# Kernel optimization log

Hardware: AMD Instinct MI355X
Metric: run time of the kernel (lower is better)

Reference implementation:

```python
import jax, jax.numpy as jnp
import numpy as np
import math

B_ = 4
L_ = 2048
D_MODEL = 1024
D_STATE = 128
D_CONV = 4
HEADDIM = 64
CHUNK = 256
D_INNER = 2 * D_MODEL
NHEADS = D_INNER // HEADDIM
CONV_DIM = D_INNER + 2 * D_STATE
D_IN_PROJ = 2 * D_INNER + 2 * D_STATE + NHEADS


def setup_inputs() -> dict:
    key = jax.random.key(0)
    ks = jax.random.split(key, 8)
    u = jax.random.normal(ks[0], (B_, L_, D_MODEL), jnp.float32)
    W_in = jax.random.normal(ks[1], (D_IN_PROJ, D_MODEL), jnp.float32) * 0.02
    conv_w = jax.random.normal(ks[2], (CONV_DIM, D_CONV), jnp.float32) * 0.2
    conv_b = jnp.zeros((CONV_DIM,), jnp.float32)
    # dt init as in the torch module: dt ~ logU(0.001, 0.1), inverse-softplus
    dt = jnp.exp(jax.random.uniform(ks[3], (NHEADS,), jnp.float32) * (math.log(0.1) - math.log(0.001)) + math.log(0.001))
    dt = jnp.clip(dt, 1e-4, None)
    dt_bias = dt + jnp.log(-jnp.expm1(-dt))
    A_log = jnp.log(jax.random.uniform(ks[4], (NHEADS,), jnp.float32, minval=1.0, maxval=1.1))
    D_param = jnp.ones((NHEADS,), jnp.float32)
    norm_w = jnp.ones((D_INNER,), jnp.float32)
    W_out = jax.random.normal(ks[5], (D_MODEL, D_INNER), jnp.float32) * 0.02
    return {"u": u, "W_in": W_in, "conv_w": conv_w, "conv_b": conv_b,
            "dt_bias": dt_bias, "A_log": A_log, "D_param": D_param,
            "norm_w": norm_w, "W_out": W_out}


def _ssd(x, dt, A, Bm, Cm):
    """Chunked SSD scan (mamba_chunk_scan_combined math, ngroups=1).
    x: (b,l,h,p)  dt: (b,l,h) post-softplus  A: (h,)  Bm/Cm: (b,l,n)."""
    b, l, h, p = x.shape
    n = Bm.shape[-1]
    nc = l // CHUNK
    xr = x.reshape(b, nc, CHUNK, h, p)
    dtr = dt.reshape(b, nc, CHUNK, h)
    Br = Bm.reshape(b, nc, CHUNK, n)
    Cr = Cm.reshape(b, nc, CHUNK, n)
    dA = dtr * A                                    # (b,nc,cs,h), negative
    dA_cs = jnp.cumsum(dA, axis=2)                  # (b,nc,cs,h)
    # intra-chunk decay L[i,j] = exp(sum_{k=j+1..i} dA_k) for i >= j else 0
    diff = dA_cs[:, :, :, None, :] - dA_cs[:, :, None, :, :]  # (b,nc,i,j,h)
    mask = jnp.tril(jnp.ones((CHUNK, CHUNK), bool))
    Lmat = jnp.exp(jnp.where(mask[None, None, :, :, None], diff, -jnp.inf))
    dtx = dtr[..., None] * xr                       # (b,nc,cs,h,p)
    Y_diag = jnp.einsum('bcin,bcjn,bcijh,bcjhp->bcihp', Cr, Br, Lmat, dtx)
    # per-chunk final states
    decay_states = jnp.exp(dA_cs[:, :, -1:, :] - dA_cs)  # (b,nc,cs,h)
    states = jnp.einsum('bcjn,bcjh,bcjhp->bchpn', Br, decay_states, dtx)
    # inter-chunk recurrence over nc
    chunk_decay = jnp.exp(dA_cs[:, :, -1, :])       # (b,nc,h)
    def step(carry, inp):
        s, d = inp
        return carry * d[:, :, None, None] + s, carry
    init = jnp.zeros((b, h, p, n), x.dtype)
    _, prev = jax.lax.scan(step, init, (jnp.moveaxis(states, 1, 0), jnp.moveaxis(chunk_decay, 1, 0)))
    prev = jnp.moveaxis(prev, 0, 1)                 # (b,nc,h,p,n): state entering each chunk
    Y_off = jnp.einsum('bcin,bchpn,bcih->bcihp', Cr, prev, jnp.exp(dA_cs))
    return (Y_diag + Y_off).reshape(b, l, h, p)


def reference(u, W_in, conv_w, conv_b, dt_bias, A_log, D_param, norm_w, W_out):
    b, l, _ = u.shape
    zxbcdt = jnp.einsum('bld,ed->ble', u, W_in)     # (b,l,d_in_proj)
    z = zxbcdt[..., :D_INNER]
    xBC = zxbcdt[..., D_INNER:D_INNER + CONV_DIM]
    dt = zxbcdt[..., D_INNER + CONV_DIM:]
    # depthwise causal conv1d + SiLU
    xt = jnp.moveaxis(xBC, 1, 2)                    # (b,c,l)
    y = jax.lax.conv_general_dilated(xt, conv_w[:, None, :], (1,), [(D_CONV - 1, 0)], feature_group_count=CONV_DIM)
    xBC = jax.nn.silu(jnp.moveaxis(y + conv_b[None, :, None], 2, 1))
    x = xBC[..., :D_INNER].reshape(b, l, NHEADS, HEADDIM)
    Bm = xBC[..., D_INNER:D_INNER + D_STATE]
    Cm = xBC[..., D_INNER + D_STATE:]
    dt = jax.nn.softplus(dt + dt_bias)
    A = -jnp.exp(A_log)
    yh = _ssd(x, dt, A, Bm, Cm) + D_param[:, None] * x
    yf = yh.reshape(b, l, D_INNER)
    # gated RMSNorm (norm_before_gate=False): norm(y * silu(z)) * w
    g = yf * jax.nn.silu(z)
    g = g * jax.lax.rsqrt(jnp.mean(g * g, axis=-1, keepdims=True) + 1e-5) * norm_w
    return jnp.einsum('bld,ed->ble', g, W_out)
```

## Files before the change

kernel.cpp:

```cpp
#include <hip/hip_runtime.h>
#include <hip/hip_bf16.h>
#include <math.h>

#define B_N     4
#define L_N     2048
#define DMODEL  1024
#define DSTATE  128
#define DCONV   4
#define HEADDIM 64
#define CHUNK   256
#define DINNER  2048
#define NHEADS  32
#define CONVDIM 2304
#define DINPROJ 4384
#define NCHUNK  8
#define BL      (B_N*L_N)

typedef unsigned short ushort_t;
typedef unsigned int   uint_t;

typedef __attribute__((ext_vector_type(8))) short bf16x8;
typedef __attribute__((ext_vector_type(4))) float f32x4;

__device__ __forceinline__ float bfbits2f(ushort_t u){
    union { uint_t i; float f; } v; v.i = ((uint_t)u) << 16; return v.f;
}
__device__ __forceinline__ ushort_t f2bf(float f){
    union { float f; uint_t i; } v; v.f = f;
    uint_t r = v.i + 0x7FFF + ((v.i >> 16) & 1);
    return (ushort_t)(r >> 16);
}
__device__ __forceinline__ void gload_lds16(const void* g, void* l){
    __builtin_amdgcn_global_load_lds(
        (const __attribute__((address_space(1))) unsigned int*)g,
        (__attribute__((address_space(3))) unsigned int*)l, 16, 0, 0);
}

__global__ __launch_bounds__(256) void cvt_bf16(
    const float* __restrict__ in, ushort_t* __restrict__ out, int n8)
{
    int i = blockIdx.x*256 + threadIdx.x;
    if (i >= n8) return;
    const float4* p = (const float4*)(in + (size_t)i*8);
    float4 a = p[0], b = p[1];
    ushort_t o[8] = { f2bf(a.x), f2bf(a.y), f2bf(a.z), f2bf(a.w),
                      f2bf(b.x), f2bf(b.y), f2bf(b.z), f2bf(b.w) };
    *(uint4*)(out + (size_t)i*8) = *(const uint4*)o;
}

__global__ __launch_bounds__(256) void cvt_wT(
    const float* __restrict__ cw, float* __restrict__ wT)
{
    int c = blockIdx.x*256 + threadIdx.x;
    if (c >= CONVDIM) return;
    float4 v = *(const float4*)&cw[c*DCONV];
    wT[0*CONVDIM + c] = v.x;
    wT[1*CONVDIM + c] = v.y;
    wT[2*CONVDIM + c] = v.z;
    wT[3*CONVDIM + c] = v.w;
}

template<int KDIM, int NTILES, int EPI>
__global__ __launch_bounds__(256) void gemm_bt_mfma(
    const ushort_t* __restrict__ A, const ushort_t* __restrict__ B,
    float* __restrict__ outf, ushort_t* __restrict__ z, ushort_t* __restrict__ xbc,
    const float* __restrict__ dt_bias, float* __restrict__ dtp)
{
    __shared__ __align__(16) ushort_t Asl[2][128*32];
    __shared__ __align__(16) ushort_t Bsl[2][128*32];

    int nwg = gridDim.x;
    int cpx = nwg >> 3;
    int lin = blockIdx.x;
    int work = (lin & 7)*cpx + (lin >> 3);
    int mtile = work / NTILES, ntile = work % NTILES;
    int m0 = mtile*128, n0 = ntile*128;

    int t = threadIdx.x;
    int l = t & 63, w = t >> 6;
    int wr = w >> 1, wc = w & 1;
    int lr16 = l & 15, kb = l >> 4;
    int srow = t >> 2, skc = (t & 3)*8;

    f32x4 acc[4][4];
    #pragma unroll
    for (int m=0;m<4;m++){
        #pragma unroll
        for (int n=0;n<4;n++) acc[m][n] = (f32x4){0.f,0.f,0.f,0.f};
    }

    int br0 = n0 + srow, br1 = n0 + 64 + srow;
    if (EPI == 1){
        br0 = (br0 < DINPROJ) ? br0 : (DINPROJ-1);
        br1 = (br1 < DINPROJ) ? br1 : (DINPROJ-1);
    }

    auto stage = [&](int buf, int k0){
        gload_lds16(A + (size_t)(m0+srow)*KDIM + k0 + skc,    &Asl[buf][t*8]);
        gload_lds16(A + (size_t)(m0+64+srow)*KDIM + k0 + skc, &Asl[buf][2048 + t*8]);
        gload_lds16(B + (size_t)br0*KDIM + k0 + skc,          &Bsl[buf][t*8]);
        gload_lds16(B + (size_t)br1*KDIM + k0 + skc,          &Bsl[buf][2048 + t*8]);
    };

    auto compute = [&](int cur){
        bf16x8 af[4], bfr[4];
        #pragma unroll
        for (int m=0;m<4;m++) af[m]  = *(const bf16x8*)&Asl[cur][(wr*64+m*16+lr16)*32 + kb*8];
        #pragma unroll
        for (int n=0;n<4;n++) bfr[n] = *(const bf16x8*)&Bsl[cur][(wc*64+n*16+lr16)*32 + kb*8];
        __builtin_amdgcn_s_setprio(1);
        #pragma unroll
        for (int m=0;m<4;m++){
            #pragma unroll
            for (int n=0;n<4;n++)
                acc[m][n] = __builtin_amdgcn_mfma_f32_16x16x32_bf16(af[m], bfr[n], acc[m][n], 0, 0, 0);
        }
        __builtin_amdgcn_s_setprio(0);
    };

    stage(0, 0);
    __syncthreads();
    int cur = 0;

    for (int k0=32; k0<KDIM; k0+=32){
        stage(cur^1, k0);
        compute(cur);
        __syncthreads();
        cur ^= 1;
    }
    compute(cur);

    #pragma unroll
    for (int m=0;m<4;m++){
        int rbase = m0 + wr*64 + m*16 + (l>>4)*4;
        #pragma unroll
        for (int n=0;n<4;n++){
            int gcol = n0 + wc*64 + n*16 + lr16;
            f32x4 v = acc[m][n];
            #pragma unroll
            for (int q=0;q<4;q++){
                int row = rbase + q;
                if (EPI == 0) {
                    outf[(size_t)row*DMODEL + gcol] = v[q];
                } else {
                    if (gcol < DINNER) {
                        z[(size_t)row*DINNER + gcol] = f2bf(v[q]);
                    } else if (gcol < DINNER + CONVDIM) {
                        xbc[(size_t)row*CONVDIM + (gcol - DINNER)] = f2bf(v[q]);
                    } else if (gcol < DINPROJ) {
                        int hh = gcol - (DINNER + CONVDIM);
                        float x = v[q] + dt_bias[hh];
                        float sp = (x > 15.f) ? x : log1pf(__expf(x));
                        int bb = row >> 11, ll = row & (L_N-1);
                        dtp[((size_t)bb*NHEADS + hh)*L_N + ll] = sp;
                    }
                }
            }
        }
    }
}

__global__ __launch_bounds__(256) void conv_silu(
    const __hip_bfloat16* __restrict__ xraw,
    const float* __restrict__ wT, const float* __restrict__ cb,
    __hip_bfloat16* __restrict__ xout)
{
    int idx = blockIdx.x*256 + threadIdx.x;
    int c8 = (idx % (CONVDIM/8))*8;
    int ml = idx / (CONVDIM/8);
    int b  = ml >> 11, l = ml & (L_N-1);
    const ushort_t* xr = (const ushort_t*)xraw;
    float acc[8];
    {
        float4 b0 = *(const float4*)&cb[c8];
        float4 b1 = *(const float4*)&cb[c8+4];
        acc[0]=b0.x; acc[1]=b0.y; acc[2]=b0.z; acc[3]=b0.w;
        acc[4]=b1.x; acc[5]=b1.y; acc[6]=b1.z; acc[7]=b1.w;
    }
    #pragma unroll
    for (int k=0;k<DCONV;k++){
        int li = l - (DCONV-1) + k;
        if (li >= 0){
            bf16x8 v = *(const bf16x8*)&xr[((size_t)b*L_N + li)*CONVDIM + c8];
            float4 w0 = *(const float4*)&wT[k*CONVDIM + c8];
            float4 w1 = *(const float4*)&wT[k*CONVDIM + c8 + 4];
            float wv[8] = {w0.x,w0.y,w0.z,w0.w,w1.x,w1.y,w1.z,w1.w};
            #pragma unroll
            for (int e=0;e<8;e++)
                acc[e] += wv[e] * bfbits2f(((const ushort_t*)&v)[e]);
        }
    }
    ushort_t o[8];
    #pragma unroll
    for (int e=0;e<8;e++){
        float s = acc[e] / (1.f + __expf(-acc[e]));
        o[e] = f2bf(s);
    }
    *(uint4*)((ushort_t*)xout + (size_t)idx*8) = *(const uint4*)o;
}

__global__ __launch_bounds__(256) void dt_cumsum(
    const float* __restrict__ dtp, const float* __restrict__ A_log,
    float* __restrict__ dAcs)
{
    int blk = blockIdx.x;
    int c  = blk % NCHUNK;
    int bh = blk / NCHUNK;
    int h  = bh & (NHEADS-1);
    int t  = threadIdx.x;
    float A = -__expf(A_log[h]);
    __shared__ float sm[CHUNK];
    float v = dtp[(size_t)bh*L_N + c*CHUNK + t] * A;
    sm[t] = v;
    __syncthreads();
    for (int off=1; off<CHUNK; off<<=1){
        float add = (t >= off) ? sm[t-off] : 0.f;
        __syncthreads();
        sm[t] += add;
        __syncthreads();
    }
    dAcs[(size_t)bh*L_N + c*CHUNK + t] = sm[t];
}

__global__ __launch_bounds__(256) void bc_scores_mfma(
    const __hip_bfloat16* __restrict__ xbc, ushort_t* __restrict__ S_T)
{
    __shared__ __align__(16) ushort_t Bs2[256*136];
    __shared__ __align__(16) ushort_t Cs2[256*136];
    int bc = blockIdx.x;
    int t = threadIdx.x;
    int l = t & 63, w = t >> 6;
    int l15 = l & 15, l4 = l >> 4;
    const ushort_t* xb = (const ushort_t*)xbc;
    const size_t rowbase = (size_t)bc*CHUNK*CONVDIM;

    #pragma unroll
    for (int ps=0; ps<16; ps++){
        int idx = ps*256 + t;
        int r = idx >> 4, ck = idx & 15;
        *(uint4*)&Bs2[r*136 + ck*8] =
            *(const uint4*)&xb[rowbase + (size_t)r*CONVDIM + DINNER + ck*8];
        *(uint4*)&Cs2[r*136 + ck*8] =
            *(const uint4*)&xb[rowbase + (size_t)r*CONVDIM + (DINNER+DSTATE) + ck*8];
    }
    __syncthreads();

    ushort_t* Sb = S_T + (size_t)bc*CHUNK*264;
    for (int if4 = w; if4 < 4; if4++){
        f32x4 acc[4][4];
        #pragma unroll
        for (int jf=0;jf<4;jf++){
            #pragma unroll
            for (int ir=0;ir<4;ir++) acc[jf][ir] = (f32x4){0.f,0.f,0.f,0.f};
        }
        #pragma unroll
        for (int k=0;k<4;k++){
            bf16x8 af[4], bfC[4];
            #pragma unroll
            for (int jf=0;jf<4;jf++)
                af[jf] = *(const bf16x8*)&Bs2[(w*64 + jf*16 + l15)*136 + k*32 + l4*8];
            #pragma unroll
            for (int ir=0;ir<4;ir++)
                bfC[ir] = *(const bf16x8*)&Cs2[(if4*64 + ir*16 + l15)*136 + k*32 + l4*8];
            #pragma unroll
            for (int jf=0;jf<4;jf++){
                #pragma unroll
                for (int ir=0;ir<4;ir++)
                    acc[jf][ir] = __builtin_amdgcn_mfma_f32_16x16x32_bf16(af[jf], bfC[ir], acc[jf][ir], 0, 0, 0);
            }
        }
        #pragma unroll
        for (int jf=0;jf<4;jf++){
            #pragma unroll
            for (int ir=0;ir<4;ir++){
                #pragma unroll
                for (int q=0;q<4;q++){
                    int j = w*64 + jf*16 + l4*4 + q;
                    int i = if4*64 + ir*16 + l15;
                    Sb[(size_t)j*264 + i] = f2bf(acc[jf][ir][q]);
                }
            }
        }
    }
}

__device__ __forceinline__ int swz264(int row, int col){
    return row*264 + (col ^ (((row>>3)&7)<<3));
}

__global__ __launch_bounds__(256) void ssd_states_mfma(
    const __hip_bfloat16* __restrict__ xbc,
    const float* __restrict__ dtp, const float* __restrict__ dAcs,
    float* __restrict__ states)
{
    __shared__ __align__(16) ushort_t xdT[64*264];
    __shared__ __align__(16) ushort_t BT[128*264];
    __shared__ float coef_s[CHUNK];
    int bc = blockIdx.x, hg = blockIdx.y;
    int b = bc >> 3, c = bc & 7;
    int t = threadIdx.x;
    int l = t & 63, w = t >> 6;
    int l15 = l & 15, l4 = l >> 4;
    const ushort_t* xb = (const ushort_t*)xbc;
    const size_t rowbase = (size_t)bc*CHUNK*CONVDIM;

    #pragma unroll
    for (int ps=0; ps<16; ps++){
        int idx = ps*256 + t;
        int j = idx >> 4, n0 = (idx & 15)*8;
        bf16x8 v = *(const bf16x8*)&xb[rowbase + (size_t)j*CONVDIM + DINNER + n0];
        #pragma unroll
        for (int e=0;e<8;e++)
            BT[swz264(n0+e, j)] = ((const ushort_t*)&v)[e];
    }

    for (int hh=0; hh<4; hh++){
        int h = hg*4 + hh;
        size_t dbase = ((size_t)b*NHEADS + h)*L_N + c*CHUNK;
        float last = dAcs[dbase + CHUNK-1];
        float cf = __expf(last - dAcs[dbase + t]) * dtp[dbase + t];
        coef_s[t] = cf;
        __syncthreads();

        #pragma unroll
        for (int ps=0; ps<8; ps++){
            int idx = ps*256 + t;
            int j = idx >> 3, p0 = (idx & 7)*8;
            float cj = coef_s[j];
            bf16x8 v = *(const bf16x8*)&xb[rowbase + (size_t)j*CONVDIM + h*HEADDIM + p0];
            #pragma unroll
            for (int e=0;e<8;e++)
                xdT[swz264(p0+e, j)] = f2bf(cj * bfbits2f(((const ushort_t*)&v)[e]));
        }
        __syncthreads();

        f32x4 acc[4][2];
        #pragma unroll
        for (int pf=0;pf<4;pf++){
            #pragma unroll
            for (int nf=0;nf<2;nf++) acc[pf][nf] = (f32x4){0.f,0.f,0.f,0.f};
        }

        #pragma unroll
        for (int k=0;k<8;k++){
            bf16x8 af[4], bv[2];
            #pragma unroll
            for (int pf=0;pf<4;pf++)
                af[pf] = *(const bf16x8*)&xdT[swz264(pf*16 + l15, k*32 + l4*8)];
            #pragma unroll
            for (int nf=0;nf<2;nf++)
                bv[nf] = *(const bf16x8*)&BT[swz264(w*32 + nf*16 + l15, k*32 + l4*8)];
            #pragma unroll
            for (int pf=0;pf<4;pf++){
                #pragma unroll
                for (int nf=0;nf<2;nf++)
                    acc[pf][nf] = __builtin_amdgcn_mfma_f32_16x16x32_bf16(af[pf], bv[nf], acc[pf][nf], 0, 0, 0);
            }
        }

        float* sb = states + (size_t)(bc*NHEADS + h)*HEADDIM*DSTATE;
        #pragma unroll
        for (int pf=0;pf<4;pf++){
            #pragma unroll
            for (int nf=0;nf<2;nf++){
                #pragma unroll
                for (int q=0;q<4;q++){
                    int p = pf*16 + l4*4 + q;
                    int n = w*32 + nf*16 + l15;
                    sb[(size_t)p*DSTATE + n] = acc[pf][nf][q];
                }
            }
        }
    }
}

__global__ __launch_bounds__(256) void scan_states(
    float* __restrict__ states, const float* __restrict__ dAcs)
{
    int idx = blockIdx.x*256 + threadIdx.x;
    int n  = idx & 127;
    int p  = (idx >> 7) & 63;
    int bh = idx >> 13;
    int b  = bh >> 5, h = bh & 31;
    float carry = 0.f;
    for (int c=0;c<NCHUNK;c++){
        size_t off = (((size_t)((b*NCHUNK + c)*NHEADS + h))*HEADDIM + p)*DSTATE + n;
        float s = states[off];
        states[off] = carry;
        float cd = __expf(dAcs[((size_t)b*NHEADS + h)*L_N + c*CHUNK + (CHUNK-1)]);
        carry = carry * cd + s;
    }
}

__global__ __launch_bounds__(256) void ssd_mfma(
    const __hip_bfloat16* __restrict__ xbc,
    const float* __restrict__ dtp, const float* __restrict__ dAcs,
    const float* __restrict__ states, const ushort_t* __restrict__ S_T,
    const float* __restrict__ D_param, ushort_t* __restrict__ yh)
{
    __shared__ __align__(16) ushort_t Ws[256*72];
    __shared__ __align__(16) ushort_t xdT[64*264];
    __shared__ float da_s[CHUNK];
    __shared__ float dt_s[CHUNK];

    int bc = blockIdx.x, h = blockIdx.y;
    int b = bc >> 3, c = bc & 7;
    int t = threadIdx.x;
    int l = t & 63, w = t >> 6;
    int l15 = l & 15, l4 = l >> 4;

    const ushort_t* xb = (const ushort_t*)xbc;
    const size_t rowbase = (size_t)bc*CHUNK*CONVDIM;

    da_s[t] = dAcs[((size_t)b*NHEADS + h)*L_N + c*CHUNK + t];
    dt_s[t] = dtp[((size_t)b*NHEADS + h)*L_N + c*CHUNK + t];

    #pragma unroll
    for (int ps=0; ps<8; ps++){
        int idx = ps*256 + t;
        int j = idx >> 3, p0 = (idx & 7)*8;
        bf16x8 v = *(const bf16x8*)&xb[rowbase + (size_t)j*CONVDIM + h*HEADDIM + p0];
        #pragma unroll
        for (int e=0;e<8;e++) xdT[(p0+e)*264 + j] = ((const ushort_t*)&v)[e];
    }
    __syncthreads();

    f32x4 yacc[4][4];
    #pragma unroll
    for (int m=0;m<4;m++){
        #pragma unroll
        for (int np=0;np<4;np++) yacc[m][np] = (f32x4){0.f,0.f,0.f,0.f};
    }

    const ushort_t* cbase = xb + rowbase + (size_t)l15*CONVDIM + (DINNER+DSTATE) + l4*8;
    const float*    pbase = states + (size_t)(bc*NHEADS + h)*HEADDIM*DSTATE
                                   + (size_t)l15*DSTATE + l4*8;
    #pragma unroll
    for (int k=0;k<4;k++){
        bf16x8 bfk[4];
        #pragma unroll
        for (int np=0;np<4;np++){
            const float* pr = pbase + (size_t)(np*16)*DSTATE + k*32;
            float4 a = *(const float4*)pr;
            float4 bq = *(const float4*)(pr + 4);
            bf16x8 r;
            r[0]=(short)f2bf(a.x);  r[1]=(short)f2bf(a.y);
            r[2]=(short)f2bf(a.z);  r[3]=(short)f2bf(a.w);
            r[4]=(short)f2bf(bq.x); r[5]=(short)f2bf(bq.y);
            r[6]=(short)f2bf(bq.z); r[7]=(short)f2bf(bq.w);
            bfk[np] = r;
        }
        #pragma unroll
        for (int m=0;m<4;m++){
            int i0 = (m*4 + w)*16;
            bf16x8 af = *(const bf16x8*)(cbase + (size_t)i0*CONVDIM + k*32);
            #pragma unroll
            for (int np=0;np<4;np++)
                yacc[m][np] = __builtin_amdgcn_mfma_f32_16x16x32_bf16(af, bfk[np], yacc[m][np], 0, 0, 0);
        }
    }
    #pragma unroll
    for (int m=0;m<4;m++){
        int i0 = (m*4 + w)*16;
        #pragma unroll
        for (int q=0;q<4;q++){
            float e = __expf(da_s[i0 + l4*4 + q]);
            #pragma unroll
            for (int np=0;np<4;np++) yacc[m][np][q] *= e;
        }
    }

    const ushort_t* Sb = S_T + (size_t)bc*CHUNK*264;
    for (int jp=0; jp<4; jp++){
        bf16x8 bfx[4][2];
        #pragma unroll
        for (int np=0;np<4;np++){
            #pragma unroll
            for (int ks=0;ks<2;ks++)
                bfx[np][ks] = *(const bf16x8*)&xdT[(np*16 + l15)*264 + jp*64 + ks*32 + l4*8];
        }

        #pragma unroll
        for (int m=0;m<4;m++){
            int i0 = (m*4 + w)*16;
            int imax = i0 + 15;
            int kmaxY = (jp*64 <= imax ? 1 : 0) + (jp*64+32 <= imax ? 1 : 0);
            if (kmaxY == 0) continue;
            int nmax = 2*kmaxY;

            float dai[4];
            #pragma unroll
            for (int q=0;q<4;q++) dai[q] = da_s[i0 + l4*4 + q];
            #pragma unroll
            for (int n=0;n<4;n++){
                if (n < nmax){
                    int jcol = jp*64 + n*16 + l15;
                    float daj = da_s[jcol], dtj = dt_s[jcol];
                    ushort_t sv[4];
                    *(uint2*)sv = *(const uint2*)&Sb[(size_t)jcol*264 + i0 + l4*4];
                    #pragma unroll
                    for (int q=0;q<4;q++){
                        int i = i0 + l4*4 + q;
                        float wv = 0.f;
                        if (jcol <= i) wv = __expf(dai[q] - daj) * dtj * bfbits2f(sv[q]);
                        Ws[i*72 + n*16 + l15] = f2bf(wv);
                    }
                }
            }
            #pragma unroll
            for (int ks=0;ks<2;ks++){
                if (ks < kmaxY){
                    bf16x8 wfA = *(const bf16x8*)&Ws[(i0 + l15)*72 + ks*32 + l4*8];
                    #pragma unroll
                    for (int np=0;np<4;np++)
                        yacc[m][np] = __builtin_amdgcn_mfma_f32_16x16x32_bf16(wfA, bfx[np][ks], yacc[m][np], 0, 0, 0);
                }
            }
        }
    }

    float Dh = D_param[h];
    #pragma unroll
    for (int m=0;m<4;m++){
        int i0 = (m*4 + w)*16;
        #pragma unroll
        for (int np=0;np<4;np++){
            int p = np*16 + l15;
            #pragma unroll
            for (int q=0;q<4;q++){
                int i = i0 + l4*4 + q;
                float xv = bfbits2f(xdT[p*264 + i]);
                yh[((size_t)bc*CHUNK + i)*DINNER + h*HEADDIM + p] = f2bf(yacc[m][np][q] + Dh*xv);
            }
        }
    }
}

__global__ __launch_bounds__(256) void gate_norm(
    const ushort_t* __restrict__ yh, const __hip_bfloat16* __restrict__ z,
    const float* __restrict__ norm_w, __hip_bfloat16* __restrict__ g)
{
    int row = blockIdx.x;
    int t = threadIdx.x;
    const ushort_t* yr = yh + (size_t)row*DINNER + t*8;
    const ushort_t* zr = (const ushort_t*)z + (size_t)row*DINNER + t*8;
    bf16x8 yv = *(const bf16x8*)yr;
    bf16x8 zv8 = *(const bf16x8*)zr;
    float v[8];
    float ss = 0.f;
    #pragma unroll
    for (int e=0;e<8;e++){
        float y = bfbits2f(((const ushort_t*)&yv)[e]);
        float zz = bfbits2f(((const ushort_t*)&zv8)[e]);
        float gv = y * (zz / (1.f + __expf(-zz)));
        v[e] = gv; ss += gv*gv;
    }
    #pragma unroll
    for (int off=32; off>=1; off>>=1) ss += __shfl_xor(ss, off);
    __shared__ float red[4];
    if ((t & 63) == 0) red[t >> 6] = ss;
    __syncthreads();
    float tot = red[0]+red[1]+red[2]+red[3];
    float scale = rsqrtf(tot * (1.f/DINNER) + 1e-5f);
    float4 w0 = *(const float4*)&norm_w[t*8];
    float4 w1 = *(const float4*)&norm_w[t*8+4];
    float nw[8] = {w0.x,w0.y,w0.z,w0.w,w1.x,w1.y,w1.z,w1.w};
    ushort_t o[8];
    #pragma unroll
    for (int e=0;e<8;e++) o[e] = f2bf(v[e]*scale*nw[e]);
    *(uint4*)((ushort_t*)g + (size_t)row*DINNER + t*8) = *(const uint4*)o;
}

extern "C" void kernel_launch(void* const* d_in, const int* in_sizes, int n_in,
                              void* d_out, int out_size, void* d_ws, size_t ws_size,
                              hipStream_t stream)
{
    const float* u       = (const float*)d_in[0];
    const float* W_in    = (const float*)d_in[1];
    const float* conv_w  = (const float*)d_in[2];
    const float* conv_b  = (const float*)d_in[3];
    const float* dt_bias = (const float*)d_in[4];
    const float* A_log   = (const float*)d_in[5];
    const float* D_param = (const float*)d_in[6];
    const float* norm_w  = (const float*)d_in[7];
    const float* W_out   = (const float*)d_in[8];
    float* out = (float*)d_out;

    char* p = (char*)d_ws;
    auto take = [&](size_t n){ char* r = p; p += (n + 255) & ~(size_t)255; return r; };

    __hip_bfloat16* z       = (__hip_bfloat16*)take((size_t)BL*DINNER*2);
    __hip_bfloat16* xbc_raw = (__hip_bfloat16*)take((size_t)BL*CONVDIM*2);
    __hip_bfloat16* xbc     = (__hip_bfloat16*)take((size_t)BL*CONVDIM*2);
    float* dtp     = (float*)take((size_t)BL*NHEADS*4);
    float* dAcs    = (float*)take((size_t)BL*NHEADS*4);
    float* states  = (float*)take((size_t)B_N*NCHUNK*NHEADS*HEADDIM*DSTATE*4);
    ushort_t* yh   = (ushort_t*)take((size_t)BL*DINNER*2);
    ushort_t* S_T  = (ushort_t*)take((size_t)B_N*NCHUNK*CHUNK*264*2);
    ushort_t* u_bf  = (ushort_t*)take((size_t)BL*DMODEL*2);
    ushort_t* Wi_bf = (ushort_t*)take((size_t)DINPROJ*DMODEL*2);
    ushort_t* Wo_bf = (ushort_t*)take((size_t)DMODEL*DINNER*2);
    float* wT       = (float*)take((size_t)DCONV*CONVDIM*4);
    __hip_bfloat16* g = z;

    cvt_bf16<<<dim3((BL*DMODEL/8 + 255)/256), 256, 0, stream>>>(u, u_bf, BL*DMODEL/8);
    cvt_bf16<<<dim3((DINPROJ*DMODEL/8 + 255)/256), 256, 0, stream>>>(W_in, Wi_bf, DINPROJ*DMODEL/8);
    cvt_bf16<<<dim3((DMODEL*DINNER/8 + 255)/256), 256, 0, stream>>>(W_out, Wo_bf, DMODEL*DINNER/8);
    cvt_wT<<<dim3((CONVDIM+255)/256), 256, 0, stream>>>(conv_w, wT);

    gemm_bt_mfma<DMODEL,35,1><<<dim3(64*35), 256, 0, stream>>>(
        u_bf, Wi_bf, nullptr, (ushort_t*)z, (ushort_t*)xbc_raw, dt_bias, dtp);

    conv_silu<<<dim3(BL*(CONVDIM/8)/256), 256, 0, stream>>>(xbc_raw, wT, conv_b, xbc);
    dt_cumsum<<<dim3(B_N*NHEADS*NCHUNK), 256, 0, stream>>>(dtp, A_log, dAcs);
    bc_scores_mfma<<<dim3(B_N*NCHUNK), 256, 0, stream>>>(xbc, S_T);
    ssd_states_mfma<<<dim3(B_N*NCHUNK, NHEADS/4), 256, 0, stream>>>(xbc, dtp, dAcs, states);
    scan_states<<<dim3((B_N*NHEADS*HEADDIM*DSTATE)/256), 256, 0, stream>>>(states, dAcs);
    ssd_mfma<<<dim3(B_N*NCHUNK, NHEADS), 256, 0, stream>>>(xbc, dtp, dAcs, states, S_T, D_param, yh);
    gate_norm<<<dim3(BL), 256, 0, stream>>>(yh, z, norm_w, g);

    gemm_bt_mfma<DINNER,8,0><<<dim3(64*8), 256, 0, stream>>>(
        (const ushort_t*)g, Wo_bf, out, nullptr, nullptr, nullptr, nullptr);
}
```

Baseline: 366.5 us.

## Replace in-projection GEMM with 256x256-tile, 512-thread, 8-phase pipelined MFMA kernel

The input-projection GEMM moves to a dedicated kernel with 256x256 output tiles, 8 waves per block, K-steps of 64 split into two 32-wide halves, and explicit vmcnt waits with raw barriers. Global-to-LDS loads for the next half-step are interleaved between MFMA groups. LDS uses an XOR-swizzled paired-row layout to avoid bank conflicts. The larger tiles raise data reuse and cut the block count, but they use much more LDS and registers, which lowers occupancy and adds padding waste on the 4384-column edge (18 tiles cover 4608 columns).

```diff
diff --git a/kernel.cpp b/kernel.cpp
--- a/kernel.cpp
+++ b/kernel.cpp
@@ -36,6 +36,12 @@
         (__attribute__((address_space(3))) unsigned int*)l, 16, 0, 0);
 }
 
+#define FENCE()  asm volatile("" ::: "memory")
+#define WAITV8() asm volatile("s_waitcnt vmcnt(8)" ::: "memory")
+#define WAITV4() asm volatile("s_waitcnt vmcnt(4)" ::: "memory")
+#define WAITV0() asm volatile("s_waitcnt vmcnt(0)" ::: "memory")
+#define BARRIER() { FENCE(); __builtin_amdgcn_s_barrier(); FENCE(); }
+
 __global__ __launch_bounds__(256) void cvt_bf16(
     const float* __restrict__ in, ushort_t* __restrict__ out, int n8)
 {
@@ -60,18 +66,213 @@
     wT[3*CONVDIM + c] = v.w;
 }
 
-template<int KDIM, int NTILES, int EPI>
+__global__ __launch_bounds__(512) void gemm_inproj_8ph(
+    const ushort_t* __restrict__ A, const ushort_t* __restrict__ B,
+    ushort_t* __restrict__ z, ushort_t* __restrict__ xbc,
+    const float* __restrict__ dt_bias, float* __restrict__ dtp)
+{
+    constexpr int KD = DMODEL;
+    constexpr int NT = KD/64;
+    constexpr int NTILES = 18;
+    __shared__ __align__(16) ushort_t Alds[2][2][128*64];
+    __shared__ __align__(16) ushort_t Blds[2][2][128*64];
+
+    int nwg = gridDim.x, cpx = nwg >> 3, lin = blockIdx.x;
+    int work = (lin & 7)*cpx + (lin >> 3);
+    int mtile = work / NTILES, ntile = work % NTILES;
+    int m0 = mtile*256, n0 = ntile*256;
+
+    int t = threadIdx.x;
+    int l = t & 63, w = t >> 6;
+    int wm = w >> 2, wn = w & 3;
+    int l15 = l & 15, l4 = l >> 4;
+
+    int s_pr8  = l >> 3;
+    int s_rlow = (l >> 2) & 1;
+    int s_lb4  = (l & 3) ^ ((l >> 3) & 3);
+
+    f32x4 acc[8][4];
+    #pragma unroll
+    for (int m=0;m<8;m++){
+        #pragma unroll
+        for (int n=0;n<4;n++) acc[m][n] = (f32x4){0.f,0.f,0.f,0.f};
+    }
+
+    auto stageA = [&](int buf,int kh,int kt,int j){
+        int region = w*2 + j;
+        int pr = region*8 + s_pr8;
+        int r  = 2*pr + s_rlow;
+        const ushort_t* src = A + (size_t)(m0 + r)*KD + kt*64 + kh*32 + s_lb4*8;
+        gload_lds16(src, &Alds[buf][kh][region*512 + l*8]);
+    };
+    auto stageB = [&](int buf,int kh,int kt,int j){
+        int region = w*2 + j;
+        int pr = region*8 + s_pr8;
+        int r  = 2*pr + s_rlow;
+        int gr = n0 + r; gr = (gr < DINPROJ) ? gr : (DINPROJ-1);
+        const ushort_t* src = B + (size_t)gr*KD + kt*64 + kh*32 + s_lb4*8;
+        gload_lds16(src, &Blds[buf][kh][region*512 + l*8]);
+    };
+    auto Afrag = [&](int buf,int kh,int m)->bf16x8{
+        int r = wm*128 + m*16 + l15;
+        int pr = r >> 1;
+        return *(const bf16x8*)&Alds[buf][kh][pr*64 + (r&1)*32 + (l4 ^ (pr&3))*8];
+    };
+    auto Bfrag = [&](int buf,int kh,int n)->bf16x8{
+        int r = wn*64 + n*16 + l15;
+        int pr = r >> 1;
+        return *(const bf16x8*)&Blds[buf][kh][pr*64 + (r&1)*32 + (l4 ^ (pr&3))*8];
+    };
+
+    stageA(0,0,0,0); stageA(0,0,0,1); stageB(0,0,0,0); stageB(0,0,0,1);
+    stageA(0,1,0,0); stageA(0,1,0,1); stageB(0,1,0,0); stageB(0,1,0,1);
+    stageA(1,0,1,0); stageA(1,0,1,1); stageB(1,0,1,0); stageB(1,0,1,1);
+
+    for (int kt = 0; kt < NT-1; ++kt){
+        int buf = kt & 1, bufo = buf ^ 1;
+        bool s2 = (kt + 2 < NT);
+        WAITV8(); BARRIER();
+        {
+            bf16x8 b0 = Bfrag(buf,0,0), b1 = Bfrag(buf,0,1), b2 = Bfrag(buf,0,2), b3 = Bfrag(buf,0,3);
+            bf16x8 a0 = Afrag(buf,0,0), a1 = Afrag(buf,0,1), a2 = Afrag(buf,0,2), a3 = Afrag(buf,0,3);
+            stageA(bufo,1,kt+1,0); stageA(bufo,1,kt+1,1);
+            __builtin_amdgcn_s_setprio(1);
+            acc[0][0]=__builtin_amdgcn_mfma_f32_16x16x32_bf16(a0,b0,acc[0][0],0,0,0);
+            acc[0][1]=__builtin_amdgcn_mfma_f32_16x16x32_bf16(a0,b1,acc[0][1],0,0,0);
+            acc[0][2]=__builtin_amdgcn_mfma_f32_16x16x32_bf16(a0,b2,acc[0][2],0,0,0);
+            acc[0][3]=__builtin_amdgcn_mfma_f32_16x16x32_bf16(a0,b3,acc[0][3],0,0,0);
+            acc[1][0]=__builtin_amdgcn_mfma_f32_16x16x32_bf16(a1,b0,acc[1][0],0,0,0);
+            acc[1][1]=__builtin_amdgcn_mfma_f32_16x16x32_bf16(a1,b1,acc[1][1],0,0,0);
+            acc[1][2]=__builtin_amdgcn_mfma_f32_16x16x32_bf16(a1,b2,acc[1][2],0,0,0);
+            acc[1][3]=__builtin_amdgcn_mfma_f32_16x16x32_bf16(a1,b3,acc[1][3],0,0,0);
+            acc[2][0]=__builtin_amdgcn_mfma_f32_16x16x32_bf16(a2,b0,acc[2][0],0,0,0);
+            acc[2][1]=__builtin_amdgcn_mfma_f32_16x16x32_bf16(a2,b1,acc[2][1],0,0,0);
+            acc[2][2]=__builtin_amdgcn_mfma_f32_16x16x32_bf16(a2,b2,acc[2][2],0,0,0);
+            acc[2][3]=__builtin_amdgcn_mfma_f32_16x16x32_bf16(a2,b3,acc[2][3],0,0,0);
+            acc[3][0]=__builtin_amdgcn_mfma_f32_16x16x32_bf16(a3,b0,acc[3][0],0,0,0);
+            acc[3][1]=__builtin_amdgcn_mfma_f32_16x16x32_bf16(a3,b1,acc[3][1],0,0,0);
+            acc[3][2]=__builtin_amdgcn_mfma_f32_16x16x32_bf16(a3,b2,acc[3][2],0,0,0);
+            acc[3][3]=__builtin_amdgcn_mfma_f32_16x16x32_bf16(a3,b3,acc[3][3],0,0,0);
+            __builtin_amdgcn_s_setprio(0);
+            bf16x8 a4 = Afrag(buf,0,4), a5 = Afrag(buf,0,5), a6 = Afrag(buf,0,6), a7 = Afrag(buf,0,7);
+            stageB(bufo,1,kt+1,0); stageB(bufo,1,kt+1,1);
+            __builtin_amdgcn_s_setprio(1);
+            acc[4][0]=__builtin_amdgcn_mfma_f32_16x16x32_bf16(a4,b0,acc[4][0],0,0,0);
+            acc[4][1]=__builtin_amdgcn_mfma_f32_16x16x32_bf16(a4,b1,acc[4][1],0,0,0);
+            acc[4][2]=__builtin_amdgcn_mfma_f32_16x16x32_bf16(a4,b2,acc[4][2],0,0,0);
+            acc[4][3]=__builtin_amdgcn_mfma_f32_16x16x32_bf16(a4,b3,acc[4][3],0,0,0);
+            acc[5][0]=__builtin_amdgcn_mfma_f32_16x16x32_bf16(a5,b0,acc[5][0],0,0,0);
+            acc[5][1]=__builtin_amdgcn_mfma_f32_16x16x32_bf16(a5,b1,acc[5][1],0,0,0);
+            acc[5][2]=__builtin_amdgcn_mfma_f32_16x16x32_bf16(a5,b2,acc[5][2],0,0,0);
+            acc[5][3]=__builtin_amdgcn_mfma_f32_16x16x32_bf16(a5,b3,acc[5][3],0,0,0);
+            acc[6][0]=__builtin_amdgcn_mfma_f32_16x16x32_bf16(a6,b0,acc[6][0],0,0,0);
+            acc[6][1]=__builtin_amdgcn_mfma_f32_16x16x32_bf16(a6,b1,acc[6][1],0,0,0);
+            acc[6][2]=__builtin_amdgcn_mfma_f32_16x16x32_bf16(a6,b2,acc[6][2],0,0,0);
+            acc[6][3]=__builtin_amdgcn_mfma_f32_16x16x32_bf16(a6,b3,acc[6][3],0,0,0);
+            acc[7][0]=__builtin_amdgcn_mfma_f32_16x16x32_bf16(a7,b0,acc[7][0],0,0,0);
+            acc[7][1]=__builtin_amdgcn_mfma_f32_16x16x32_bf16(a7,b1,acc[7][1],0,0,0);
+            acc[7][2]=__builtin_amdgcn_mfma_f32_16x16x32_bf16(a7,b2,acc[7][2],0,0,0);
+            acc[7][3]=__builtin_amdgcn_mfma_f32_16x16x32_bf16(a7,b3,acc[7][3],0,0,0);
+            __builtin_amdgcn_s_setprio(0);
+        }
+        WAITV8(); BARRIER();
+        {
+            bf16x8 b0 = Bfrag(buf,1,0), b1 = Bfrag(buf,1,1), b2 = Bfrag(buf,1,2), b3 = Bfrag(buf,1,3);
+            bf16x8 a0 = Afrag(buf,1,0), a1 = Afrag(buf,1,1), a2 = Afrag(buf,1,2), a3 = Afrag(buf,1,3);
+            if (s2){ stageA(buf,0,kt+2,0); stageA(buf,0,kt+2,1); }
+            __builtin_amdgcn_s_setprio(1);
+            acc[0][0]=__builtin_amdgcn_mfma_f32_16x16x32_bf16(a0,b0,acc[0][0],0,0,0);
+            acc[0][1]=__builtin_amdgcn_mfma_f32_16x16x32_bf16(a0,b1,acc[0][1],0,0,0);
+            acc[0][2]=__builtin_amdgcn_mfma_f32_16x16x32_bf16(a0,b2,acc[0][2],0,0,0);
+            acc[0][3]=__builtin_amdgcn_mfma_f32_16x16x32_bf16(a0,b3,acc[0][3],0,0,0);
+            acc[1][0]=__builtin_amdgcn_mfma_f32_16x16x32_bf16(a1,b0,acc[1][0],0,0,0);
+            acc[1][1]=__builtin_amdgcn_mfma_f32_16x16x32_bf16(a1,b1,acc[1][1],0,0,0);
+            acc[1][2]=__builtin_amdgcn_mfma_f32_16x16x32_bf16(a1,b2,acc[1][2],0,0,0);
+            acc[1][3]=__builtin_amdgcn_mfma_f32_16x16x32_bf16(a1,b3,acc[1][3],0,0,0);
+            acc[2][0]=__builtin_amdgcn_mfma_f32_16x16x32_bf16(a2,b0,acc[2][0],0,0,0);
+            acc[2][1]=__builtin_amdgcn_mfma_f32_16x16x32_bf16(a2,b1,acc[2][1],0,0,0);
+            acc[2][2]=__builtin_amdgcn_mfma_f32_16x16x32_bf16(a2,b2,acc[2][2],0,0,0);
+            acc[2][3]=__builtin_amdgcn_mfma_f32_16x16x32_bf16(a2,b3,acc[2][3],0,0,0);
+            acc[3][0]=__builtin_amdgcn_mfma_f32_16x16x32_bf16(a3,b0,acc[3][0],0,0,0);
+            acc[3][1]=__builtin_amdgcn_mfma_f32_16x16x32_bf16(a3,b1,acc[3][1],0,0,0);
+            acc[3][2]=__builtin_amdgcn_mfma_f32_16x16x32_bf16(a3,b2,acc[3][2],0,0,0);
+            acc[3][3]=__builtin_amdgcn_mfma_f32_16x16x32_bf16(a3,b3,acc[3][3],0,0,0);
+            __builtin_amdgcn_s_setprio(0);
+            bf16x8 a4 = Afrag(buf,1,4), a5 = Afrag(buf,1,5), a6 = Afrag(buf,1,6), a7 = Afrag(buf,1,7);
+            if (s2){ stageB(buf,0,kt+2,0); stageB(buf,0,kt+2,1); }
+            __builtin_amdgcn_s_setprio(1);
+            acc[4][0]=__builtin_amdgcn_mfma_f32_16x16x32_bf16(a4,b0,acc[4][0],0,0,0);
+            acc[4][1]=__builtin_amdgcn_mfma_f32_16x16x32_bf16(a4,b1,acc[4][1],0,0,0);
+            acc[4][2]=__builtin_amdgcn_mfma_f32_16x16x32_bf16(a4,b2,acc[4][2],0,0,0);
+            acc[4][3]=__builtin_amdgcn_mfma_f32_16x16x32_bf16(a4,b3,acc[4][3],0,0,0);
+            acc[5][0]=__builtin_amdgcn_mfma_f32_16x16x32_bf16(a5,b0,acc[5][0],0,0,0);
+            acc[5][1]=__builtin_amdgcn_mfma_f32_16x16x32_bf16(a5,b1,acc[5][1],0,0,0);
+            acc[5][2]=__builtin_amdgcn_mfma_f32_16x16x32_bf16(a5,b2,acc[5][2],0,0,0);
+            acc[5][3]=__builtin_amdgcn_mfma_f32_16x16x32_bf16(a5,b3,acc[5][3],0,0,0);
+            acc[6][0]=__builtin_amdgcn_mfma_f32_16x16x32_bf16(a6,b0,acc[6][0],0,0,0);
+            acc[6][1]=__builtin_amdgcn_mfma_f32_16x16x32_bf16(a6,b1,acc[6][1],0,0,0);
+            acc[6][2]=__builtin_amdgcn_mfma_f32_16x16x32_bf16(a6,b2,acc[6][2],0,0,0);
+            acc[6][3]=__builtin_amdgcn_mfma_f32_16x16x32_bf16(a6,b3,acc[6][3],0,0,0);
+            acc[7][0]=__builtin_amdgcn_mfma_f32_16x16x32_bf16(a7,b0,acc[7][0],0,0,0);
+            acc[7][1]=__builtin_amdgcn_mfma_f32_16x16x32_bf16(a7,b1,acc[7][1],0,0,0);
+            acc[7][2]=__builtin_amdgcn_mfma_f32_16x16x32_bf16(a7,b2,acc[7][2],0,0,0);
+            acc[7][3]=__builtin_amdgcn_mfma_f32_16x16x32_bf16(a7,b3,acc[7][3],0,0,0);
+            __builtin_amdgcn_s_setprio(0);
+        }
+    }
+    {
+        int buf = (NT-1) & 1;
+        WAITV4(); BARRIER();
+        #pragma unroll
+        for (int kh=0; kh<2; kh++){
+            if (kh == 1){ WAITV0(); BARRIER(); }
+            bf16x8 b0 = Bfrag(buf,kh,0), b1 = Bfrag(buf,kh,1), b2 = Bfrag(buf,kh,2), b3 = Bfrag(buf,kh,3);
+            #pragma unroll
+            for (int m=0;m<8;m++){
+                bf16x8 a = Afrag(buf,kh,m);
+                acc[m][0]=__builtin_amdgcn_mfma_f32_16x16x32_bf16(a,b0,acc[m][0],0,0,0);
+                acc[m][1]=__builtin_amdgcn_mfma_f32_16x16x32_bf16(a,b1,acc[m][1],0,0,0);
+                acc[m][2]=__builtin_amdgcn_mfma_f32_16x16x32_bf16(a,b2,acc[m][2],0,0,0);
+                acc[m][3]=__builtin_amdgcn_mfma_f32_16x16x32_bf16(a,b3,acc[m][3],0,0,0);
+            }
+        }
+    }
+
+    #pragma unroll
+    for (int m=0;m<8;m++){
+        int rbase = m0 + wm*128 + m*16 + l4*4;
+        #pragma unroll
+        for (int n=0;n<4;n++){
+            int gcol = n0 + wn*64 + n*16 + l15;
+            f32x4 v = acc[m][n];
+            #pragma unroll
+            for (int q=0;q<4;q++){
+                int row = rbase + q;
+                if (gcol < DINNER) {
+                    z[(size_t)row*DINNER + gcol] = f2bf(v[q]);
+                } else if (gcol < DINNER + CONVDIM) {
+                    xbc[(size_t)row*CONVDIM + (gcol - DINNER)] = f2bf(v[q]);
+                } else if (gcol < DINPROJ) {
+                    int hh = gcol - (DINNER + CONVDIM);
+                    float x = v[q] + dt_bias[hh];
+                    float sp = (x > 15.f) ? x : log1pf(__expf(x));
+                    int bb = row >> 11, ll = row & (L_N-1);
+                    dtp[((size_t)bb*NHEADS + hh)*L_N + ll] = sp;
+                }
+            }
+        }
+    }
+}
+
+template<int KDIM, int NTILES>
 __global__ __launch_bounds__(256) void gemm_bt_mfma(
     const ushort_t* __restrict__ A, const ushort_t* __restrict__ B,
-    float* __restrict__ outf, ushort_t* __restrict__ z, ushort_t* __restrict__ xbc,
-    const float* __restrict__ dt_bias, float* __restrict__ dtp)
+    float* __restrict__ outf)
 {
     __shared__ __align__(16) ushort_t Asl[2][128*32];
     __shared__ __align__(16) ushort_t Bsl[2][128*32];
 
-    int nwg = gridDim.x;
-    int cpx = nwg >> 3;
-    int lin = blockIdx.x;
+    int nwg = gridDim.x, cpx = nwg >> 3, lin = blockIdx.x;
     int work = (lin & 7)*cpx + (lin >> 3);
     int mtile = work / NTILES, ntile = work % NTILES;
     int m0 = mtile*128, n0 = ntile*128;
@@ -89,19 +290,12 @@
         for (int n=0;n<4;n++) acc[m][n] = (f32x4){0.f,0.f,0.f,0.f};
     }
 
-    int br0 = n0 + srow, br1 = n0 + 64 + srow;
-    if (EPI == 1){
-        br0 = (br0 < DINPROJ) ? br0 : (DINPROJ-1);
-        br1 = (br1 < DINPROJ) ? br1 : (DINPROJ-1);
-    }
-
     auto stage = [&](int buf, int k0){
         gload_lds16(A + (size_t)(m0+srow)*KDIM + k0 + skc,    &Asl[buf][t*8]);
         gload_lds16(A + (size_t)(m0+64+srow)*KDIM + k0 + skc, &Asl[buf][2048 + t*8]);
-        gload_lds16(B + (size_t)br0*KDIM + k0 + skc,          &Bsl[buf][t*8]);
-        gload_lds16(B + (size_t)br1*KDIM + k0 + skc,          &Bsl[buf][2048 + t*8]);
+        gload_lds16(B + (size_t)(n0+srow)*KDIM + k0 + skc,    &Bsl[buf][t*8]);
+        gload_lds16(B + (size_t)(n0+64+srow)*KDIM + k0 + skc, &Bsl[buf][2048 + t*8]);
     };
-
     auto compute = [&](int cur){
         bf16x8 af[4], bfr[4];
         #pragma unroll
@@ -121,7 +315,6 @@
     stage(0, 0);
     __syncthreads();
     int cur = 0;
-
     for (int k0=32; k0<KDIM; k0+=32){
         stage(cur^1, k0);
         compute(cur);
@@ -138,24 +331,8 @@
             int gcol = n0 + wc*64 + n*16 + lr16;
             f32x4 v = acc[m][n];
             #pragma unroll
-            for (int q=0;q<4;q++){
-                int row = rbase + q;
-                if (EPI == 0) {
-                    outf[(size_t)row*DMODEL + gcol] = v[q];
-                } else {
-                    if (gcol < DINNER) {
-                        z[(size_t)row*DINNER + gcol] = f2bf(v[q]);
-                    } else if (gcol < DINNER + CONVDIM) {
-                        xbc[(size_t)row*CONVDIM + (gcol - DINNER)] = f2bf(v[q]);
-                    } else if (gcol < DINPROJ) {
-                        int hh = gcol - (DINNER + CONVDIM);
-                        float x = v[q] + dt_bias[hh];
-                        float sp = (x > 15.f) ? x : log1pf(__expf(x));
-                        int bb = row >> 11, ll = row & (L_N-1);
-                        dtp[((size_t)bb*NHEADS + hh)*L_N + ll] = sp;
-                    }
-                }
-            }
+            for (int q=0;q<4;q++)
+                outf[(size_t)(rbase+q)*DMODEL + gcol] = v[q];
         }
     }
 }
@@ -608,8 +785,8 @@
     cvt_bf16<<<dim3((DMODEL*DINNER/8 + 255)/256), 256, 0, stream>>>(W_out, Wo_bf, DMODEL*DINNER/8);
     cvt_wT<<<dim3((CONVDIM+255)/256), 256, 0, stream>>>(conv_w, wT);
 
-    gemm_bt_mfma<DMODEL,35,1><<<dim3(64*35), 256, 0, stream>>>(
-        u_bf, Wi_bf, nullptr, (ushort_t*)z, (ushort_t*)xbc_raw, dt_bias, dtp);
+    gemm_inproj_8ph<<<dim3(32*18), 512, 0, stream>>>(
+        u_bf, Wi_bf, (ushort_t*)z, (ushort_t*)xbc_raw, dt_bias, dtp);
 
     conv_silu<<<dim3(BL*(CONVDIM/8)/256), 256, 0, stream>>>(xbc_raw, wT, conv_b, xbc);
     dt_cumsum<<<dim3(B_N*NHEADS*NCHUNK), 256, 0, stream>>>(dtp, A_log, dAcs);
@@ -619,6 +796,6 @@
     ssd_mfma<<<dim3(B_N*NCHUNK, NHEADS), 256, 0, stream>>>(xbc, dtp, dAcs, states, S_T, D_param, yh);
     gate_norm<<<dim3(BL), 256, 0, stream>>>(yh, z, norm_w, g);
 
-    gemm_bt_mfma<DINNER,8,0><<<dim3(64*8), 256, 0, stream>>>(
-        (const ushort_t*)g, Wo_bf, out, nullptr, nullptr, nullptr, nullptr);
-}
+    gemm_bt_mfma<DINNER,8><<<dim3(64*8), 256, 0, stream>>>(
+        (const ushort_t*)g, Wo_bf, out);
+}
```

Measured after the change: 403.0 us. 9.9% more time.
